# Performance work log

Measured on AMD Instinct MI355X. Metric: run time of the kernel, lower is better.

Reference implementation:

```python
import jax, jax.numpy as jnp
import numpy as np
from jax.experimental import sparse as jsparse

N_ITEMS = 20000   # item catalog size (S is [N_ITEMS, N_ITEMS])
N_USERS = 2048    # user batch
NNZ = 4_000_000


def setup_inputs() -> dict:
    key = jax.random.key(0)
    k1, k2, k3, k4 = jax.random.split(key, 4)
    X = jax.random.normal(k1, (N_USERS, N_ITEMS), dtype=jnp.float32)
    S_vals = jax.random.normal(k2, (NNZ,), dtype=jnp.float32)
    S_rows = jax.random.randint(k3, (NNZ,), 0, N_ITEMS, dtype=jnp.int32)
    S_cols = jax.random.randint(k4, (NNZ,), 0, N_ITEMS, dtype=jnp.int32)
    return {"X": X, "S_vals": S_vals, "S_rows": S_rows, "S_cols": S_cols}


def reference(X, S_vals, S_rows, S_cols):
    # torch.sparse.mm(S, X.t()).t()  ==  X @ S^T, with S sparse COO.
    indices = jnp.stack([S_rows, S_cols], axis=1)  # [nnz, 2]
    S = jsparse.BCOO((S_vals, indices), shape=(N_ITEMS, N_ITEMS))
    # (S @ X^T)^T -> [n_users, n_items]; duplicate indices sum, matching COO semantics.
    return (S @ X.T).T
```

## Files before the change

### kernel.cpp

```cpp
#include <hip/hip_runtime.h>

#define N_ITEMS 20000
#define N_USERS 2048
#define NNZ     4000000
#define LDP     2112
#define CAP     320

typedef float f32x4 __attribute__((ext_vector_type(4)));

#define OFF_XT     ((size_t)0)
#define OFF_CSRPK  ((size_t)84480000)
#define OFF_CNT    (OFF_CSRPK + 25600000)

static __device__ __forceinline__ unsigned short f2bf(float f) {
  unsigned u = __float_as_uint(f);
  unsigned r = (u + 0x7fffu + ((u >> 16) & 1u)) >> 16;
  return (unsigned short)r;
}

#define NT_BLOCKS (313 * 32)
#define NS_BLOCKS ((NNZ / 4 + 255) / 256)

__global__ __launch_bounds__(256) void prep_kernel(
    const float* __restrict__ X, const float* __restrict__ vals,
    const int* __restrict__ rows, const int* __restrict__ cols,
    unsigned short* __restrict__ XT, int* __restrict__ cnt,
    unsigned* __restrict__ csr_pk) {
  int b = blockIdx.x;
  if (b < NT_BLOCKS) {
    __shared__ float tile[64][65];
    int k0 = (b % 313) * 64;
    int u0 = (b / 313) * 64;
    int lane = threadIdx.x & 63;
    int dq = threadIdx.x >> 6;
    #pragma unroll
    for (int m = 0; m < 16; ++m) {
      int u = u0 + dq + 4 * m;
      int k = k0 + lane;
      float v = 0.f;
      if (k < N_ITEMS) v = X[(size_t)u * N_ITEMS + k];
      tile[lane][dq + 4 * m] = v;
    }
    __syncthreads();
    #pragma unroll
    for (int m = 0; m < 16; ++m) {
      int k = k0 + dq + 4 * m;
      if (k < N_ITEMS)
        XT[(size_t)k * LDP + u0 + lane] = f2bf(tile[dq + 4 * m][lane]);
    }
  } else {
    int i = ((b - NT_BLOCKS) * 256 + threadIdx.x) * 4;
    if (i < NNZ) {
      int4   r4 = *reinterpret_cast<const int4*>(rows + i);
      int4   c4 = *reinterpret_cast<const int4*>(cols + i);
      float4 v4 = *reinterpret_cast<const float4*>(vals + i);
      #pragma unroll
      for (int k = 0; k < 4; ++k) {
        int   r = (k == 0) ? r4.x : (k == 1) ? r4.y : (k == 2) ? r4.z : r4.w;
        int   c = (k == 0) ? c4.x : (k == 1) ? c4.y : (k == 2) ? c4.z : c4.w;
        float v = (k == 0) ? v4.x : (k == 1) ? v4.y : (k == 2) ? v4.z : v4.w;
        int pos = atomicAdd(&cnt[r], 1);
        if (pos >= CAP) pos = CAP - 1;
        csr_pk[r * CAP + pos] = ((unsigned)f2bf(v) << 16) | (unsigned)c;
      }
    }
  }
}

__global__ __launch_bounds__(256) void spmm_kernel(
    const int* __restrict__ cnt, const unsigned* __restrict__ csr_pk,
    const unsigned short* __restrict__ xt, float* __restrict__ out) {
  __shared__ float tile[16][132];
  int wg = blockIdx.x;
  int xcd = wg & 7;
  int slot = wg >> 3;
  int combo = slot / 1250;
  int rb = slot - combo * 1250;
  int uchunk = xcd * 2 + combo;
  int u0 = uchunk * 128;
  int r0 = rb * 16;
  int lane = threadIdx.x & 63;
  int wave = __builtin_amdgcn_readfirstlane((int)(threadIdx.x >> 6));
  const char* xtb = (const char*)(xt + u0) + 4 * lane;

#define LOAD8(E, BASE)                                                   \
  { _Pragma("unroll")                                                    \
    for (int k = 0; k < 8; ++k) E[k] = csr_pk[(BASE) + k]; }
#define GATHER8(G, E)                                                    \
  { _Pragma("unroll")                                                    \
    for (int k = 0; k < 8; ++k)                                          \
      G[k] = *reinterpret_cast<const unsigned*>(                         \
          xtb + (E[k] & 0xffffu) * (LDP * 2)); }
#define FMA8(G, E)                                                       \
  { _Pragma("unroll")                                                    \
    for (int k = 0; k < 8; ++k) {                                        \
      float v  = __uint_as_float(E[k]);            \
      float xl = __uint_as_float(G[k] << 16);                            \
      float xh = __uint_as_float(G[k]);            \
      if (k & 1) { a2 = fmaf(v, xl, a2); a3 = fmaf(v, xh, a3); }         \
      else       { a0 = fmaf(v, xl, a0); a1 = fmaf(v, xh, a1); }         \
    } }

  #pragma unroll 1
  for (int rr = 0; rr < 4; ++rr) {
    int r = r0 + wave * 4 + rr;
    int jb = r * CAP;
    int cr = __builtin_amdgcn_readfirstlane(cnt[r]);
    if (cr > CAP) cr = CAP;
    int nb = (cr + 7) >> 3;
    float a0 = 0.f, a1 = 0.f, a2 = 0.f, a3 = 0.f;
    if (nb >= 2) {
      unsigned e0[8], e1[8], g0[8], g1[8];
      LOAD8(e0, jb)
      GATHER8(g0, e0)
      LOAD8(e1, jb + 8)
      int b = 0;
      for (; b + 3 < nb; b += 2) {
        GATHER8(g1, e1)
        FMA8(g0, e0)
        LOAD8(e0, jb + (b + 2) * 8)
        GATHER8(g0, e0)
        FMA8(g1, e1)
        LOAD8(e1, jb + (b + 3) * 8)
      }
      GATHER8(g1, e1)
      FMA8(g0, e0)
      if (nb - b == 3) {
        LOAD8(e0, jb + (b + 2) * 8)
        GATHER8(g0, e0)
        FMA8(g1, e1)
        FMA8(g0, e0)
      } else {
        FMA8(g1, e1)
      }
    } else if (nb == 1) {
      unsigned e0[8], g0[8];
      LOAD8(e0, jb)
      GATHER8(g0, e0)
      FMA8(g0, e0)
    }
    tile[wave * 4 + rr][2 * lane]     = a0 + a2;
    tile[wave * 4 + rr][2 * lane + 1] = a1 + a3;
  }
#undef LOAD8
#undef GATHER8
#undef FMA8

  __syncthreads();
  int ul = threadIdx.x >> 1;
  int rseg = (threadIdx.x & 1) * 8;
  float* op = &out[(size_t)(u0 + ul) * N_ITEMS + r0 + rseg];
  f32x4 o0, o1;
  o0.x = tile[rseg + 0][ul]; o0.y = tile[rseg + 1][ul];
  o0.z = tile[rseg + 2][ul]; o0.w = tile[rseg + 3][ul];
  o1.x = tile[rseg + 4][ul]; o1.y = tile[rseg + 5][ul];
  o1.z = tile[rseg + 6][ul]; o1.w = tile[rseg + 7][ul];
  __builtin_nontemporal_store(o0, reinterpret_cast<f32x4*>(op));
  __builtin_nontemporal_store(o1, reinterpret_cast<f32x4*>(op) + 1);
}

extern "C" void kernel_launch(void* const* d_in, const int* in_sizes, int n_in,
                              void* d_out, int out_size, void* d_ws, size_t ws_size,
                              hipStream_t stream) {
  const float* X      = (const float*)d_in[0];
  const float* S_vals = (const float*)d_in[1];
  const int*   S_rows = (const int*)d_in[2];
  const int*   S_cols = (const int*)d_in[3];
  float* out = (float*)d_out;

  char* ws = (char*)d_ws;
  unsigned short* XT = (unsigned short*)(ws + OFF_XT);
  unsigned* csr_pk   = (unsigned*)(ws + OFF_CSRPK);
  int* cnt           = (int*)(ws + OFF_CNT);

  hipMemsetAsync(cnt, 0, N_ITEMS * sizeof(int), stream);
  hipMemsetAsync(csr_pk, 0, (size_t)N_ITEMS * CAP * sizeof(unsigned), stream);
  prep_kernel<<<NT_BLOCKS + NS_BLOCKS, 256, 0, stream>>>(
      X, S_vals, S_rows, S_cols, XT, cnt, csr_pk);
  spmm_kernel<<<1250 * 16, 256, 0, stream>>>(cnt, csr_pk, XT, out);
}
```

Baseline: 1.039 ms.

## Triple-buffer SpMM gather pipeline, vectorize CSR loads, swap packed field order

Deepens the software pipeline in the SpMM row loop from two to three in-flight gather batches, so more independent X loads are outstanding per wave to hide gather latency. CSR entry loads become two 128-bit vector loads instead of eight scalar loads. The packed entry layout now puts the column in the high half and the bf16 value in the low half, with the lane offset added after the column multiply. The deeper pipeline needs more VGPRs, which could lower occupancy.

```diff
diff --git a/kernel.cpp b/kernel.cpp
--- a/kernel.cpp
+++ b/kernel.cpp
@@ -6,7 +6,8 @@
 #define LDP     2112
 #define CAP     320
 
-typedef float f32x4 __attribute__((ext_vector_type(4)));
+typedef float    f32x4 __attribute__((ext_vector_type(4)));
+typedef unsigned u32x4 __attribute__((ext_vector_type(4)));
 
 #define OFF_XT     ((size_t)0)
 #define OFF_CSRPK  ((size_t)84480000)
@@ -61,7 +62,7 @@
         float v = (k == 0) ? v4.x : (k == 1) ? v4.y : (k == 2) ? v4.z : v4.w;
         int pos = atomicAdd(&cnt[r], 1);
         if (pos >= CAP) pos = CAP - 1;
-        csr_pk[r * CAP + pos] = ((unsigned)f2bf(v) << 16) | (unsigned)c;
+        csr_pk[r * CAP + pos] = ((unsigned)c << 16) | (unsigned)f2bf(v);
       }
     }
   }
@@ -81,22 +82,25 @@
   int r0 = rb * 16;
   int lane = threadIdx.x & 63;
   int wave = __builtin_amdgcn_readfirstlane((int)(threadIdx.x >> 6));
-  const char* xtb = (const char*)(xt + u0) + 4 * lane;
+  const char* xtb = (const char*)(xt + u0);
+  unsigned lane4 = 4 * (unsigned)lane;
 
 #define LOAD8(E, BASE)                                                   \
-  { _Pragma("unroll")                                                    \
-    for (int k = 0; k < 8; ++k) E[k] = csr_pk[(BASE) + k]; }
+  { u32x4 q0 = *reinterpret_cast<const u32x4*>(csr_pk + (BASE));         \
+    u32x4 q1 = *reinterpret_cast<const u32x4*>(csr_pk + (BASE) + 4);     \
+    E[0] = q0.x; E[1] = q0.y; E[2] = q0.z; E[3] = q0.w;                  \
+    E[4] = q1.x; E[5] = q1.y; E[6] = q1.z; E[7] = q1.w; }
 #define GATHER8(G, E)                                                    \
   { _Pragma("unroll")                                                    \
     for (int k = 0; k < 8; ++k)                                          \
       G[k] = *reinterpret_cast<const unsigned*>(                         \
-          xtb + (E[k] & 0xffffu) * (LDP * 2)); }
+          xtb + ((E[k] >> 16) * (unsigned)(LDP * 2) + lane4)); }
 #define FMA8(G, E)                                                       \
   { _Pragma("unroll")                                                    \
     for (int k = 0; k < 8; ++k) {                                        \
-      float v  = __uint_as_float(E[k]);            \
+      float v  = __uint_as_float(E[k] << 16);            \
       float xl = __uint_as_float(G[k] << 16);                            \
-      float xh = __uint_as_float(G[k]);            \
+      float xh = __uint_as_float(G[k]);             \
       if (k & 1) { a2 = fmaf(v, xl, a2); a3 = fmaf(v, xh, a3); }         \
       else       { a0 = fmaf(v, xl, a0); a1 = fmaf(v, xh, a1); }         \
     } }
@@ -109,30 +113,55 @@
     if (cr > CAP) cr = CAP;
     int nb = (cr + 7) >> 3;
     float a0 = 0.f, a1 = 0.f, a2 = 0.f, a3 = 0.f;
-    if (nb >= 2) {
+    if (nb >= 3) {
+      unsigned e0[8], e1[8], e2[8], g0[8], g1[8], g2[8];
+      LOAD8(e0, jb)
+      GATHER8(g0, e0)
+      LOAD8(e1, jb + 8)
+      GATHER8(g1, e1)
+      LOAD8(e2, jb + 16)
+      int b = 0;
+      for (; b + 5 < nb; b += 3) {
+        GATHER8(g2, e2)
+        FMA8(g0, e0)
+        LOAD8(e0, jb + (b + 3) * 8)
+        GATHER8(g0, e0)
+        FMA8(g1, e1)
+        LOAD8(e1, jb + (b + 4) * 8)
+        GATHER8(g1, e1)
+        FMA8(g2, e2)
+        LOAD8(e2, jb + (b + 5) * 8)
+      }
+      int m = nb - b;
+      GATHER8(g2, e2)
+      FMA8(g0, e0)
+      if (m == 3) {
+        FMA8(g1, e1)
+        FMA8(g2, e2)
+      } else if (m == 4) {
+        LOAD8(e0, jb + (b + 3) * 8)
+        GATHER8(g0, e0)
+        FMA8(g1, e1)
+        FMA8(g2, e2)
+        FMA8(g0, e0)
+      } else {
+        LOAD8(e0, jb + (b + 3) * 8)
+        GATHER8(g0, e0)
+        FMA8(g1, e1)
+        LOAD8(e1, jb + (b + 4) * 8)
+        GATHER8(g1, e1)
+        FMA8(g2, e2)
+        FMA8(g0, e0)
+        FMA8(g1, e1)
+      }
+    } else if (nb == 2) {
       unsigned e0[8], e1[8], g0[8], g1[8];
       LOAD8(e0, jb)
       GATHER8(g0, e0)
       LOAD8(e1, jb + 8)
-      int b = 0;
-      for (; b + 3 < nb; b += 2) {
-        GATHER8(g1, e1)
-        FMA8(g0, e0)
-        LOAD8(e0, jb + (b + 2) * 8)
-        GATHER8(g0, e0)
-        FMA8(g1, e1)
-        LOAD8(e1, jb + (b + 3) * 8)
-      }
       GATHER8(g1, e1)
       FMA8(g0, e0)
-      if (nb - b == 3) {
-        LOAD8(e0, jb + (b + 2) * 8)
-        GATHER8(g0, e0)
-        FMA8(g1, e1)
-        FMA8(g0, e0)
-      } else {
-        FMA8(g1, e1)
-      }
+      FMA8(g1, e1)
     } else if (nb == 1) {
       unsigned e0[8], g0[8];
       LOAD8(e0, jb)
```

Result: slower. 1.092 ms (+5.1%).

## Split SpMM by column half and user chunk into four passes for gather locality

Applied to the files above, without the earlier changes.

Nonzeros are binned by row and by which half of the item range their column falls in. The SpMM then runs as four launches, one per (user-chunk, column-half) pair, so each pass gathers from only half of the bf16 transposed X, a smaller working set that fits cache better. The second half pass reads the partial output back and accumulates into it, which adds extra output read and write traffic and extra launches. The packed entry format is also swapped (column in the high bits) and the CSR entries are now loaded as nontemporal 128-bit vectors.

```diff
diff --git a/kernel.cpp b/kernel.cpp
--- a/kernel.cpp
+++ b/kernel.cpp
@@ -4,13 +4,15 @@
 #define N_USERS 2048
 #define NNZ     4000000
 #define LDP     2112
-#define CAP     320
-
-typedef float f32x4 __attribute__((ext_vector_type(4)));
+#define HALF_ITEMS 10000
+#define CAP_H   192
+
+typedef float    f32x4 __attribute__((ext_vector_type(4)));
+typedef unsigned u32x4 __attribute__((ext_vector_type(4)));
 
 #define OFF_XT     ((size_t)0)
 #define OFF_CSRPK  ((size_t)84480000)
-#define OFF_CNT    (OFF_CSRPK + 25600000)
+#define OFF_CNT    (OFF_CSRPK + 30720000)
 
 static __device__ __forceinline__ unsigned short f2bf(float f) {
   unsigned u = __float_as_uint(f);
@@ -59,9 +61,12 @@
         int   r = (k == 0) ? r4.x : (k == 1) ? r4.y : (k == 2) ? r4.z : r4.w;
         int   c = (k == 0) ? c4.x : (k == 1) ? c4.y : (k == 2) ? c4.z : c4.w;
         float v = (k == 0) ? v4.x : (k == 1) ? v4.y : (k == 2) ? v4.z : v4.w;
-        int pos = atomicAdd(&cnt[r], 1);
-        if (pos >= CAP) pos = CAP - 1;
-        csr_pk[r * CAP + pos] = ((unsigned)f2bf(v) << 16) | (unsigned)c;
+        int h = (c >= HALF_ITEMS) ? 1 : 0;
+        int bin = 2 * r + h;
+        int pos = atomicAdd(&cnt[bin], 1);
+        if (pos >= CAP_H) pos = CAP_H - 1;
+        csr_pk[bin * CAP_H + pos] =
+            ((unsigned)(c - h * HALF_ITEMS) << 16) | (unsigned)f2bf(v);
       }
     }
   }
@@ -69,46 +74,64 @@
 
 __global__ __launch_bounds__(256) void spmm_kernel(
     const int* __restrict__ cnt, const unsigned* __restrict__ csr_pk,
-    const unsigned short* __restrict__ xt, float* __restrict__ out) {
-  __shared__ float tile[16][132];
+    const unsigned short* __restrict__ xt, float* __restrict__ out,
+    int uc, int h) {
+  __shared__ float tile[8][132];
   int wg = blockIdx.x;
   int xcd = wg & 7;
-  int slot = wg >> 3;
-  int combo = slot / 1250;
-  int rb = slot - combo * 1250;
-  int uchunk = xcd * 2 + combo;
-  int u0 = uchunk * 128;
-  int r0 = rb * 16;
+  int rb = wg >> 3;
+  int u0 = (xcd * 2 + uc) * 128;
+  int r0 = rb * 8;
   int lane = threadIdx.x & 63;
   int wave = __builtin_amdgcn_readfirstlane((int)(threadIdx.x >> 6));
-  const char* xtb = (const char*)(xt + u0) + 4 * lane;
-
-#define LOAD8(E, BASE)                                                   \
-  { _Pragma("unroll")                                                    \
-    for (int k = 0; k < 8; ++k) E[k] = csr_pk[(BASE) + k]; }
-#define GATHER8(G, E)                                                    \
-  { _Pragma("unroll")                                                    \
-    for (int k = 0; k < 8; ++k)                                          \
-      G[k] = *reinterpret_cast<const unsigned*>(                         \
-          xtb + (E[k] & 0xffffu) * (LDP * 2)); }
-#define FMA8(G, E)                                                       \
-  { _Pragma("unroll")                                                    \
-    for (int k = 0; k < 8; ++k) {                                        \
-      float v  = __uint_as_float(E[k]);            \
-      float xl = __uint_as_float(G[k] << 16);                            \
-      float xh = __uint_as_float(G[k]);            \
-      if (k & 1) { a2 = fmaf(v, xl, a2); a3 = fmaf(v, xh, a3); }         \
-      else       { a0 = fmaf(v, xl, a0); a1 = fmaf(v, xh, a1); }         \
+  unsigned lane4 = 4 * (unsigned)lane;
+  const char* xtb = (const char*)(xt + (size_t)h * HALF_ITEMS * LDP + u0);
+  int ul = threadIdx.x >> 1;
+  int rhalf = (threadIdx.x & 1) * 4;
+  float* op = out + (size_t)(u0 + ul) * N_ITEMS + r0 + rhalf;
+
+#define LOAD8(E, BASE)                                                       \
+  { u32x4 q0 = __builtin_nontemporal_load(                                   \
+        reinterpret_cast<const u32x4*>(csr_pk + (BASE)));                    \
+    u32x4 q1 = __builtin_nontemporal_load(                                   \
+        reinterpret_cast<const u32x4*>(csr_pk + (BASE) + 4));                \
+    E[0] = q0.x; E[1] = q0.y; E[2] = q0.z; E[3] = q0.w;                      \
+    E[4] = q1.x; E[5] = q1.y; E[6] = q1.z; E[7] = q1.w; }
+#define GATHER8(G, E)                                                        \
+  { _Pragma("unroll")                                                        \
+    for (int k = 0; k < 8; ++k)                                              \
+      G[k] = *reinterpret_cast<const unsigned*>(                             \
+          xtb + ((E[k] >> 16) * (unsigned)(LDP * 2) + lane4)); }
+#define FMA8(G, E)                                                           \
+  { _Pragma("unroll")                                                        \
+    for (int k = 0; k < 8; ++k) {                                            \
+      float v  = __uint_as_float(E[k] << 16);                \
+      float xl = __uint_as_float(G[k] << 16);                                \
+      float xh = __uint_as_float(G[k]);                 \
+      if (k & 1) { a2 = fmaf(v, xl, a2); a3 = fmaf(v, xh, a3); }             \
+      else       { a0 = fmaf(v, xl, a0); a1 = fmaf(v, xh, a1); }             \
     } }
 
+  if (h) {
+    f32x4 i0 = __builtin_nontemporal_load(reinterpret_cast<const f32x4*>(op));
+    tile[rhalf + 0][ul] = i0.x; tile[rhalf + 1][ul] = i0.y;
+    tile[rhalf + 2][ul] = i0.z; tile[rhalf + 3][ul] = i0.w;
+    __syncthreads();
+  }
+
   #pragma unroll 1
-  for (int rr = 0; rr < 4; ++rr) {
-    int r = r0 + wave * 4 + rr;
-    int jb = r * CAP;
-    int cr = __builtin_amdgcn_readfirstlane(cnt[r]);
-    if (cr > CAP) cr = CAP;
+  for (int rr = 0; rr < 2; ++rr) {
+    int r = r0 + wave * 2 + rr;
+    int bin = 2 * r + h;
+    int jb = bin * CAP_H;
+    int cr = __builtin_amdgcn_readfirstlane(cnt[bin]);
+    if (cr > CAP_H) cr = CAP_H;
     int nb = (cr + 7) >> 3;
     float a0 = 0.f, a1 = 0.f, a2 = 0.f, a3 = 0.f;
+    if (h) {
+      a0 = tile[wave * 2 + rr][2 * lane];
+      a1 = tile[wave * 2 + rr][2 * lane + 1];
+    }
     if (nb >= 2) {
       unsigned e0[8], e1[8], g0[8], g1[8];
       LOAD8(e0, jb)
@@ -139,24 +162,18 @@
       GATHER8(g0, e0)
       FMA8(g0, e0)
     }
-    tile[wave * 4 + rr][2 * lane]     = a0 + a2;
-    tile[wave * 4 + rr][2 * lane + 1] = a1 + a3;
+    tile[wave * 2 + rr][2 * lane]     = a0 + a2;
+    tile[wave * 2 + rr][2 * lane + 1] = a1 + a3;
   }
 #undef LOAD8
 #undef GATHER8
 #undef FMA8
 
   __syncthreads();
-  int ul = threadIdx.x >> 1;
-  int rseg = (threadIdx.x & 1) * 8;
-  float* op = &out[(size_t)(u0 + ul) * N_ITEMS + r0 + rseg];
-  f32x4 o0, o1;
-  o0.x = tile[rseg + 0][ul]; o0.y = tile[rseg + 1][ul];
-  o0.z = tile[rseg + 2][ul]; o0.w = tile[rseg + 3][ul];
-  o1.x = tile[rseg + 4][ul]; o1.y = tile[rseg + 5][ul];
-  o1.z = tile[rseg + 6][ul]; o1.w = tile[rseg + 7][ul];
-  __builtin_nontemporal_store(o0, reinterpret_cast<f32x4*>(op));
-  __builtin_nontemporal_store(o1, reinterpret_cast<f32x4*>(op) + 1);
+  f32x4 o;
+  o.x = tile[rhalf + 0][ul]; o.y = tile[rhalf + 1][ul];
+  o.z = tile[rhalf + 2][ul]; o.w = tile[rhalf + 3][ul];
+  __builtin_nontemporal_store(o, reinterpret_cast<f32x4*>(op));
 }
 
 extern "C" void kernel_launch(void* const* d_in, const int* in_sizes, int n_in,
@@ -173,9 +190,11 @@
   unsigned* csr_pk   = (unsigned*)(ws + OFF_CSRPK);
   int* cnt           = (int*)(ws + OFF_CNT);
 
-  hipMemsetAsync(cnt, 0, N_ITEMS * sizeof(int), stream);
-  hipMemsetAsync(csr_pk, 0, (size_t)N_ITEMS * CAP * sizeof(unsigned), stream);
+  hipMemsetAsync(cnt, 0, 2 * N_ITEMS * sizeof(int), stream);
+  hipMemsetAsync(csr_pk, 0, (size_t)2 * N_ITEMS * CAP_H * sizeof(unsigned), stream);
   prep_kernel<<<NT_BLOCKS + NS_BLOCKS, 256, 0, stream>>>(
       X, S_vals, S_rows, S_cols, XT, cnt, csr_pk);
-  spmm_kernel<<<1250 * 16, 256, 0, stream>>>(cnt, csr_pk, XT, out);
-}
+  for (int p = 0; p < 4; ++p)
+    spmm_kernel<<<2500 * 8, 256, 0, stream>>>(cnt, csr_pk, XT, out,
+                                              p >> 1, p & 1);
+}
```

After: 1.088 ms. +4.8%, slower.
